# Performance work log

Hardware: AMD Instinct MI355X
Metric: run time of the kernel (lower is better)

Reference implementation:

```python
import jax, jax.numpy as jnp
import numpy as np

B, T, C = 256, 512, 128


def setup_inputs() -> dict:
    key = jax.random.key(0)
    k1, k2, k3 = jax.random.split(key, 3)
    inputs = jax.random.normal(k1, (B, T, C), dtype=jnp.float32)
    # learned transition matrix (orthogonal init approximated by scaled normal)
    transitions = jax.random.normal(k2, (C, C), dtype=jnp.float32) * 0.1
    # variable sequence lengths in [T//2, T] -> keras-style boolean mask
    lengths = jax.random.randint(k3, (B,), T // 2, T + 1)
    mask = jnp.arange(T)[None, :] < lengths[:, None]  # [B, T] bool
    return {"inputs": inputs, "mask": mask, "transitions": transitions}


def reference(inputs, mask, transitions):
    # Faithful port of CRF.call: sequence_lengths from mask, then Viterbi decode
    # (tfa.text.crf_decode): max-plus forward DP with backpointers + backtrack.
    Bn, Tn, Cn = inputs.shape
    seq_len = jnp.sum(mask.astype(jnp.int32), axis=-1)  # [B]

    ident = jnp.arange(Cn, dtype=jnp.int32)[None, :]  # identity backpointer row

    def fwd_step(state, xs):
        # state: [B, C] best score ending in each tag
        pot_t, valid = xs  # [B, C], [B] bool
        scores = state[:, :, None] + transitions[None]      # [B, Cprev, Ccur]
        new_state = jnp.max(scores, axis=1) + pot_t          # [B, C]
        bp = jnp.argmax(scores, axis=1).astype(jnp.int32)    # [B, C]
        state = jnp.where(valid[:, None], new_state, state)  # carry past length
        bp = jnp.where(valid[:, None], bp, ident)            # identity beyond length
        return state, bp

    pots = jnp.swapaxes(inputs[:, 1:], 0, 1)  # [T-1, B, C]
    valid = mask[:, 1:].T                      # [T-1, B]
    state, bps = jax.lax.scan(fwd_step, inputs[:, 0], (pots, valid))

    last_tag = jnp.argmax(state, axis=-1).astype(jnp.int32)  # [B]

    def bwd_step(tag, bp_t):
        prev = jnp.take_along_axis(bp_t, tag[:, None], axis=1)[:, 0]
        return prev, prev

    _, tags_rest = jax.lax.scan(bwd_step, last_tag, bps, reverse=True)  # [T-1, B]
    viterbi = jnp.concatenate([tags_rest, last_tag[None]], axis=0).T    # [B, T]
    return viterbi, inputs, seq_len, transitions
```

## Files before the change

### kernel.cpp

```cpp
#include <hip/hip_runtime.h>


#define BB 256
#define TT 512
#define CC 128
#define NTH 1024
#define GR 8
#define JP 16
#define SPAD 20

#define OFF_VIT 0
#define OFF_INP (BB * TT)
#define OFF_LEN (OFF_INP + BB * TT * CC)
#define OFF_TR (OFF_LEN + BB)

#define BP_BYTES ((TT - 1) * CC)
#define STATE_FLOATS (2 * GR * SPAD)
#define SMEM_BYTES (BP_BYTES + STATE_FLOATS * 4 + 16 * 4 + 16)

#define F3(a, b, c) fmaxf(fmaxf((a), (b)), (c))

template <int C>
__device__ __forceinline__ float dppmaxf(float v) {
  float o = __int_as_float(__builtin_amdgcn_update_dpp(0, __float_as_int(v), C, 0xF, 0xF, true));
  return fmaxf(v, o);
}
template <int C>
__device__ __forceinline__ unsigned dppminu(unsigned v) {
  unsigned o = (unsigned)__builtin_amdgcn_update_dpp(0, (int)v, C, 0xF, 0xF, true);
  return v < o ? v : o;
}

__device__ __forceinline__ void lexmax(float& v, int& i, float ov, int oi) {
  bool take = (ov > v) || (ov == v && oi < i);
  v = take ? ov : v;
  i = take ? oi : i;
}
template <int C>
__device__ __forceinline__ void bfly_dpp(float& v, int& i) {
  float ov = __int_as_float(__builtin_amdgcn_update_dpp(0, __float_as_int(v), C, 0xF, 0xF, true));
  int oi = __builtin_amdgcn_update_dpp(0, i, C, 0xF, 0xF, true);
  lexmax(v, i, ov, oi);
}
__device__ __forceinline__ void bfly6(float& v, int& i) {
  bfly_dpp<0xB1>(v, i);
  bfly_dpp<0x4E>(v, i);
  bfly_dpp<0x141>(v, i);
  bfly_dpp<0x140>(v, i);
  { float ov = __shfl_xor(v, 16); int oi = __shfl_xor(i, 16); lexmax(v, i, ov, oi); }
  { float ov = __shfl_xor(v, 32); int oi = __shfl_xor(i, 32); lexmax(v, i, ov, oi); }
}

__global__ __launch_bounds__(NTH, 1) void crf_viterbi(
    const float* __restrict__ inputs, const unsigned char* __restrict__ mask_bytes,
    const float* __restrict__ trans, float* __restrict__ out) {
  extern __shared__ unsigned char smem[];
  unsigned char* bp_s = smem;
  float* state_s = (float*)(smem + BP_BYTES);
  int* wsum = (int*)(state_s + STATE_FLOATS);

  const int b = blockIdx.x;
  const int tid = threadIdx.x;
  const int lane = tid & 63;
  const int wave = tid >> 6;
  const int ccur = tid >> 3;
  const int g = tid & 7;
  const bool g0 = (g == 0);

  const int w4 = (mask_bytes[1] == 0) ? 4 : 1;
  if (tid < TT) {
    int mb = mask_bytes[(size_t)(b * TT + tid) * (size_t)w4] != 0;
    unsigned long long bal = __ballot(mb);
    if (lane == 0) wsum[wave] = __popcll(bal);
  }

  float tr[JP];
#pragma unroll
  for (int j = 0; j < JP; ++j) tr[j] = trans[(g * JP + j) * CC + ccur];

  const float* pin = inputs + (size_t)b * TT * CC;

  if (tid < CC) state_s[(tid >> 4) * SPAD + (tid & 15)] = pin[tid];
  __syncthreads();

  int L = 0;
#pragma unroll
  for (int i = 0; i < 8; ++i) L += wsum[i];

  float pot = g0 ? pin[CC + ccur] : 0.f;
  int par = 0;

  for (int t = 1; t < L; ++t) {
    const float4* sp = (const float4*)(state_s + par * (GR * SPAD) + g * SPAD);
    float4 a0 = sp[0], a1 = sp[1], a2 = sp[2], a3 = sp[3];

    int tn = (t + 1 < L) ? (t + 1) : t;
    float potN = 0.f;
    if (g0) potN = pin[tn * CC + ccur];

    float t0 = a0.x + tr[0], t1 = a0.y + tr[1], t2 = a0.z + tr[2], t3 = a0.w + tr[3];
    float t4 = a1.x + tr[4], t5 = a1.y + tr[5], t6 = a1.z + tr[6], t7 = a1.w + tr[7];
    float t8 = a2.x + tr[8], t9 = a2.y + tr[9], tA = a2.z + tr[10], tB = a2.w + tr[11];
    float tC = a3.x + tr[12], tD = a3.y + tr[13], tE = a3.z + tr[14], tF = a3.w + tr[15];

    float m = fmaxf(F3(F3(t0, t1, t2), F3(t3, t4, t5), F3(t6, t7, t8)),
                    F3(F3(t9, tA, tB), F3(tC, tD, tE), tF));
    m = dppmaxf<0xB1>(m);
    m = dppmaxf<0x4E>(m);
    m = dppmaxf<0x141>(m);

    unsigned iA = 255u, iB = 255u;
    iA = (t7 == m) ? 7u : iA;  iB = (tF == m) ? 15u : iB;
    iA = (t6 == m) ? 6u : iA;  iB = (tE == m) ? 14u : iB;
    iA = (t5 == m) ? 5u : iA;  iB = (tD == m) ? 13u : iB;
    iA = (t4 == m) ? 4u : iA;  iB = (tC == m) ? 12u : iB;
    iA = (t3 == m) ? 3u : iA;  iB = (tB == m) ? 11u : iB;
    iA = (t2 == m) ? 2u : iA;  iB = (tA == m) ? 10u : iB;
    iA = (t1 == m) ? 1u : iA;  iB = (t9 == m) ? 9u : iB;
    iA = (t0 == m) ? 0u : iA;  iB = (t8 == m) ? 8u : iB;
    unsigned bi = ((iA != 255u) ? iA : iB) + (unsigned)(g * JP);
    bi = dppminu<0xB1>(bi);
    bi = dppminu<0x4E>(bi);
    bi = dppminu<0x141>(bi);

    if (g0) {
      state_s[(par ^ 1) * (GR * SPAD) + (ccur >> 4) * SPAD + (ccur & 15)] = m + pot;
      bp_s[(t - 1) * CC + ccur] = (unsigned char)bi;
    }
    pot = potN;
    asm volatile("s_waitcnt lgkmcnt(0)\n\ts_barrier" ::: "memory");
    par ^= 1;
  }

  float* outv = out + OFF_VIT + b * TT;

  if (wave == 0) {
    const float* fs = state_s + par * (GR * SPAD);
    float v1 = fs[(lane >> 4) * SPAD + (lane & 15)];
    int c2 = lane + 64;
    float v2 = fs[(c2 >> 4) * SPAD + (c2 & 15)];
    float v;
    int idx;
    if (v2 > v1) { v = v2; idx = c2; } else { v = v1; idx = lane; }
    bfly6(v, idx);

    for (int t2 = L - 1 + lane; t2 < TT; t2 += 64) outv[t2] = (float)idx;
    if (lane == 0) {
      out[OFF_LEN + b] = (float)L;
      int cur = idx;
      for (int tt = L - 2; tt >= 0; --tt) {
        cur = bp_s[tt * CC + cur];
        outv[tt] = (float)cur;
      }
    }
  } else {
    if (wave == 1) out[OFF_TR + b * 64 + lane] = trans[b * 64 + lane];
    const float4* src = (const float4*)pin;
    float4* dst = (float4*)(out + OFF_INP + (size_t)b * TT * CC);
    for (int i = tid - 64; i < TT * CC / 4; i += NTH - 64) dst[i] = src[i];
  }
}

extern "C" void kernel_launch(void* const* d_in, const int* in_sizes, int n_in,
                              void* d_out, int out_size, void* d_ws, size_t ws_size,
                              hipStream_t stream) {
  const float* inputs = (const float*)d_in[0];
  const unsigned char* mask = (const unsigned char*)d_in[1];
  const float* trans = (const float*)d_in[2];
  float* out = (float*)d_out;

  crf_viterbi<<<BB, NTH, SMEM_BYTES, stream>>>(inputs, mask, trans, out);
}
```

Before: 440.3 us.

## Defer backpointer argmax to next step and unroll DP loop by two

The backpointer index search for step t is moved after the barrier, so it overlaps with the state loads of step t+1 and drops off the critical path between barriers. The loop is unrolled by two with fixed ping-pong offsets, and potentials are prefetched two steps ahead through a pointer. The cost is higher register pressure from keeping the previous step's 17 scores live. The L=1 edge case now runs an extra step, which may be inconsistent.

```diff
diff --git a/kernel.cpp b/kernel.cpp
--- a/kernel.cpp
+++ b/kernel.cpp
@@ -51,6 +51,54 @@
   { float ov = __shfl_xor(v, 32); int oi = __shfl_xor(i, 32); lexmax(v, i, ov, oi); }
 }
 
+#define DO_BP                                                                  \
+  {                                                                            \
+    unsigned iA = 255u, iB = 255u;                                             \
+    iA = (s7 == sm) ? 7u : iA;  iB = (sF == sm) ? 15u : iB;                    \
+    iA = (s6 == sm) ? 6u : iA;  iB = (sE == sm) ? 14u : iB;                    \
+    iA = (s5 == sm) ? 5u : iA;  iB = (sD == sm) ? 13u : iB;                    \
+    iA = (s4 == sm) ? 4u : iA;  iB = (sC == sm) ? 12u : iB;                    \
+    iA = (s3 == sm) ? 3u : iA;  iB = (sB == sm) ? 11u : iB;                    \
+    iA = (s2 == sm) ? 2u : iA;  iB = (sA == sm) ? 10u : iB;                    \
+    iA = (s1 == sm) ? 1u : iA;  iB = (s9 == sm) ? 9u : iB;                     \
+    iA = (s0 == sm) ? 0u : iA;  iB = (s8 == sm) ? 8u : iB;                     \
+    unsigned bi = ((iA != 255u) ? iA : iB) + gbase;                            \
+    bi = dppminu<0xB1>(bi);                                                    \
+    bi = dppminu<0x4E>(bi);                                                    \
+    bi = dppminu<0x141>(bi);                                                   \
+    if (g0) *bpw = (unsigned char)bi;                                          \
+    bpw += CC;                                                                 \
+  }
+
+#define STEP(ROFF, WOFF, SH)                                                   \
+  {                                                                            \
+    const float4* rp_ = (const float4*)(state_s + (ROFF) + g * SPAD);          \
+    float4 a0 = rp_[0], a1 = rp_[1], a2 = rp_[2], a3 = rp_[3];                 \
+    float potB = 0.f;                                                          \
+    if (g0) potB = prow2[ccur];                                                \
+    prow2 = (prow2 < prowLast) ? prow2 + CC : prow2;                           \
+    if (SH) DO_BP                                                              \
+    float t0 = a0.x + tr[0], t1 = a0.y + tr[1], t2 = a0.z + tr[2],             \
+          t3 = a0.w + tr[3];                                                   \
+    float t4 = a1.x + tr[4], t5 = a1.y + tr[5], t6 = a1.z + tr[6],             \
+          t7 = a1.w + tr[7];                                                   \
+    float t8 = a2.x + tr[8], t9 = a2.y + tr[9], tA = a2.z + tr[10],            \
+          tB = a2.w + tr[11];                                                  \
+    float tC = a3.x + tr[12], tD = a3.y + tr[13], tE = a3.z + tr[14],          \
+          tF = a3.w + tr[15];                                                  \
+    float m = fmaxf(F3(F3(t0, t1, t2), F3(t3, t4, t5), F3(t6, t7, t8)),        \
+                    F3(F3(t9, tA, tB), F3(tC, tD, tE), tF));                   \
+    m = dppmaxf<0xB1>(m);                                                      \
+    m = dppmaxf<0x4E>(m);                                                      \
+    m = dppmaxf<0x141>(m);                                                     \
+    if (g0) *(state_s + (WOFF) + wslot) = m + pot;                             \
+    pot = potA; potA = potB;                                                   \
+    s0 = t0; s1 = t1; s2 = t2; s3 = t3; s4 = t4; s5 = t5; s6 = t6; s7 = t7;    \
+    s8 = t8; s9 = t9; sA = tA; sB = tB; sC = tC; sD = tD; sE = tE; sF = tF;    \
+    sm = m;                                                                    \
+    asm volatile("s_waitcnt lgkmcnt(0)\n\ts_barrier" ::: "memory");            \
+  }
+
 __global__ __launch_bounds__(NTH, 1) void crf_viterbi(
     const float* __restrict__ inputs, const unsigned char* __restrict__ mask_bytes,
     const float* __restrict__ trans, float* __restrict__ out) {
@@ -66,6 +114,8 @@
   const int ccur = tid >> 3;
   const int g = tid & 7;
   const bool g0 = (g == 0);
+  const unsigned gbase = (unsigned)(g * JP);
+  const int wslot = (ccur >> 4) * SPAD + (ccur & 15);
 
   const int w4 = (mask_bytes[1] == 0) ? 4 : 1;
   if (tid < TT) {
@@ -87,55 +137,33 @@
 #pragma unroll
   for (int i = 0; i < 8; ++i) L += wsum[i];
 
-  float pot = g0 ? pin[CC + ccur] : 0.f;
-  int par = 0;
-
-  for (int t = 1; t < L; ++t) {
-    const float4* sp = (const float4*)(state_s + par * (GR * SPAD) + g * SPAD);
-    float4 a0 = sp[0], a1 = sp[1], a2 = sp[2], a3 = sp[3];
-
-    int tn = (t + 1 < L) ? (t + 1) : t;
-    float potN = 0.f;
-    if (g0) potN = pin[tn * CC + ccur];
-
-    float t0 = a0.x + tr[0], t1 = a0.y + tr[1], t2 = a0.z + tr[2], t3 = a0.w + tr[3];
-    float t4 = a1.x + tr[4], t5 = a1.y + tr[5], t6 = a1.z + tr[6], t7 = a1.w + tr[7];
-    float t8 = a2.x + tr[8], t9 = a2.y + tr[9], tA = a2.z + tr[10], tB = a2.w + tr[11];
-    float tC = a3.x + tr[12], tD = a3.y + tr[13], tE = a3.z + tr[14], tF = a3.w + tr[15];
-
-    float m = fmaxf(F3(F3(t0, t1, t2), F3(t3, t4, t5), F3(t6, t7, t8)),
-                    F3(F3(t9, tA, tB), F3(tC, tD, tE), tF));
-    m = dppmaxf<0xB1>(m);
-    m = dppmaxf<0x4E>(m);
-    m = dppmaxf<0x141>(m);
-
-    unsigned iA = 255u, iB = 255u;
-    iA = (t7 == m) ? 7u : iA;  iB = (tF == m) ? 15u : iB;
-    iA = (t6 == m) ? 6u : iA;  iB = (tE == m) ? 14u : iB;
-    iA = (t5 == m) ? 5u : iA;  iB = (tD == m) ? 13u : iB;
-    iA = (t4 == m) ? 4u : iA;  iB = (tC == m) ? 12u : iB;
-    iA = (t3 == m) ? 3u : iA;  iB = (tB == m) ? 11u : iB;
-    iA = (t2 == m) ? 2u : iA;  iB = (tA == m) ? 10u : iB;
-    iA = (t1 == m) ? 1u : iA;  iB = (t9 == m) ? 9u : iB;
-    iA = (t0 == m) ? 0u : iA;  iB = (t8 == m) ? 8u : iB;
-    unsigned bi = ((iA != 255u) ? iA : iB) + (unsigned)(g * JP);
-    bi = dppminu<0xB1>(bi);
-    bi = dppminu<0x4E>(bi);
-    bi = dppminu<0x141>(bi);
-
-    if (g0) {
-      state_s[(par ^ 1) * (GR * SPAD) + (ccur >> 4) * SPAD + (ccur & 15)] = m + pot;
-      bp_s[(t - 1) * CC + ccur] = (unsigned char)bi;
-    }
-    pot = potN;
-    asm volatile("s_waitcnt lgkmcnt(0)\n\ts_barrier" ::: "memory");
-    par ^= 1;
-  }
+  float pot = 0.f, potA = 0.f;
+  if (g0) {
+    pot = pin[CC + ccur];
+    potA = pin[2 * CC + ccur];
+  }
+  const float* prow2 = pin + 3 * CC;
+  const float* prowLast = pin + (size_t)(L - 1) * CC;
+
+  float s0, s1, s2, s3, s4, s5, s6, s7, s8, s9, sA, sB, sC, sD, sE, sF, sm;
+  unsigned char* bpw = bp_s + ccur;
+
+  STEP(0, GR * SPAD, 0);
+  int t = 2;
+  for (; t + 1 < L; t += 2) {
+    STEP(GR * SPAD, 0, 1);
+    STEP(0, GR * SPAD, 1);
+  }
+  if (t < L) {
+    STEP(GR * SPAD, 0, 1);
+  }
+  DO_BP
+  asm volatile("s_waitcnt lgkmcnt(0)\n\ts_barrier" ::: "memory");
 
   float* outv = out + OFF_VIT + b * TT;
 
   if (wave == 0) {
-    const float* fs = state_s + par * (GR * SPAD);
+    const float* fs = state_s + ((L - 1) & 1) * (GR * SPAD);
     float v1 = fs[(lane >> 4) * SPAD + (lane & 15)];
     int c2 = lane + 64;
     float v2 = fs[(c2 >> 4) * SPAD + (c2 & 15)];
```

After: 411.0 us. -6.7%, faster.
